# Kernel tuning notes

Measured on AMD Instinct MI355X. Metric: run time of the kernel, lower is better.

## Reference

```python
import jax, jax.numpy as jnp
import numpy as np

N, E, IN, HID, ADIM, EDIM, H = 20000, 320000, 128, 128, 16, 16, 2


def _lin(key, out_d, in_d, scale=0.05):
    kw, kb = jax.random.split(key)
    W = jax.random.normal(kw, (out_d, in_d), jnp.float32) * scale
    b = jax.random.normal(kb, (out_d,), jnp.float32) * scale
    return W, b


def _gat_params(key):
    k = jax.random.split(key, 4)
    Wl, bl = _lin(k[0], H * HID, HID)
    Wr, br = _lin(k[1], H * HID, HID)
    We = jax.random.normal(k[2], (H * HID, EDIM), jnp.float32) * 0.05  # lin_edge, no bias
    att = jax.random.normal(k[3], (1, H, HID), jnp.float32) * 0.05
    bias = jnp.zeros((HID,), jnp.float32)  # concat=False -> out bias of size HID
    return Wl, bl, Wr, br, We, att, bias


def setup_inputs() -> dict:
    key = jax.random.key(0)
    ks = jax.random.split(key, 16)
    inp = {}
    inp['x'] = jax.random.normal(ks[0], (N, IN), jnp.float32)
    inp['edge_index'] = jax.random.randint(ks[1], (2, E), 0, N, jnp.int64 if jax.config.jax_enable_x64 else jnp.int32)
    inp['edge_attr'] = jax.random.normal(ks[2], (E, EDIM), jnp.float32)
    inp['action'] = jax.random.normal(ks[3], (N, ADIM), jnp.float32)
    inp['inp_W'], inp['inp_b'] = _lin(ks[4], HID, IN)
    for i, name in enumerate(['s1', 's2', 'sa']):
        Wl, bl, Wr, br, We, att, bias = _gat_params(ks[5 + i])
        inp[f'{name}_Wl'], inp[f'{name}_bl'] = Wl, bl
        inp[f'{name}_Wr'], inp[f'{name}_br'] = Wr, br
        inp[f'{name}_We'], inp[f'{name}_att'], inp[f'{name}_bias'] = We, att, bias
    inp['ap_W'], inp['ap_b'] = _lin(ks[8], HID, ADIM)
    inp['g_W'], inp['g_b'] = _lin(ks[9], HID, HID)
    inp['be_W'], inp['be_b'] = _lin(ks[10], HID, HID)
    inp['q1_W'], inp['q1_b'] = _lin(ks[11], HID, HID)
    inp['q2_W'], inp['q2_b'] = _lin(ks[12], 1, HID)
    return inp


def gatv2(h, src, dst, ea, Wl, bl, Wr, br, We, att, bias):
    """PyG GATv2Conv, heads=H, concat=False (mean over heads), with edge_attr."""
    n = h.shape[0]
    xl = (h @ Wl.T + bl).reshape(n, H, HID)   # source transform
    xr = (h @ Wr.T + br).reshape(n, H, HID)   # destination transform
    em = (ea @ We.T).reshape(-1, H, HID)      # [E,H,C]
    m = jax.nn.leaky_relu(xl[src] + xr[dst] + em, 0.2)   # [E,H,C]
    logit = (m * att).sum(-1)                 # [E,H]
    lmax = jax.ops.segment_max(logit, dst, num_segments=n)
    w = jnp.exp(logit - lmax[dst])
    den = jax.ops.segment_sum(w, dst, num_segments=n)
    alpha = w / den[dst]                      # segment softmax over incoming edges
    out = jax.ops.segment_sum(alpha[..., None] * xl[src], dst, num_segments=n)  # [n,H,C]
    return out.mean(axis=1) + bias


def reference(x, edge_index, edge_attr, action, inp_W, inp_b,
              s1_Wl, s1_bl, s1_Wr, s1_br, s1_We, s1_att, s1_bias,
              s2_Wl, s2_bl, s2_Wr, s2_br, s2_We, s2_att, s2_bias,
              sa_Wl, sa_bl, sa_Wr, sa_br, sa_We, sa_att, sa_bias,
              ap_W, ap_b, g_W, g_b, be_W, be_b, q1_W, q1_b, q2_W, q2_b):
    src, dst = edge_index[0], edge_index[1]
    h = jax.nn.relu(x @ inp_W.T + inp_b)
    h = jax.nn.relu(gatv2(h, src, dst, edge_attr, s1_Wl, s1_bl, s1_Wr, s1_br, s1_We, s1_att, s1_bias))
    h = jax.nn.relu(gatv2(h, src, dst, edge_attr, s2_Wl, s2_bl, s2_Wr, s2_br, s2_We, s2_att, s2_bias))
    a = jax.nn.relu(action @ ap_W.T + ap_b)
    h = (a @ g_W.T + g_b) * h + (a @ be_W.T + be_b)   # FiLM modulation
    h = jax.nn.relu(gatv2(h, src, dst, edge_attr, sa_Wl, sa_bl, sa_Wr, sa_br, sa_We, sa_att, sa_bias))
    h = jax.nn.relu(h @ q1_W.T + q1_b)
    q_node = h @ q2_W.T + q2_b                         # [N,1]
    return q_node.mean(axis=0, keepdims=True)          # [1,1]
```

## Files before the change

### kernel.cpp

```cpp
#include <hip/hip_runtime.h>
#include <hip/hip_bf16.h>


typedef __attribute__((ext_vector_type(8))) short bf16x8;
typedef __attribute__((ext_vector_type(4))) float f32x4;
typedef __attribute__((ext_vector_type(2))) float f32x2;

#define ZERO8 ((bf16x8){0, 0, 0, 0, 0, 0, 0, 0})

__device__ __forceinline__ unsigned short f2bf(float f) {
    union { float f; unsigned int i; } v; v.f = f;
    unsigned int x = v.i;
    x += 0x7fffu + ((x >> 16) & 1u);
    return (unsigned short)(x >> 16);
}
__device__ __forceinline__ unsigned char f2fp8(float f) {
    return (unsigned char)(__builtin_amdgcn_cvt_pk_fp8_f32(f, f, 0, false) & 0xFF);
}
__device__ __forceinline__ void wave_lds_fence() {
    __builtin_amdgcn_wave_barrier();
    asm volatile("s_waitcnt lgkmcnt(0)" ::: "memory");
    __builtin_amdgcn_wave_barrier();
}

#define MAXCVT 16
struct CvtDescs {
    const float* src[MAXCVT];
    unsigned short* dst[MAXCVT];
    int off4[MAXCVT + 1];
    int cnt;
    int* deg; int ndeg4;
    int* ctr; float* col;
};
__global__ __launch_bounds__(256) void cvt_many_kernel(CvtDescs d) {
    const int tid = blockIdx.x * blockDim.x + threadIdx.x;
    const int stride = gridDim.x * blockDim.x;
    const int total = d.off4[d.cnt];
    for (int i = tid; i < total; i += stride) {
        int e = 0;
        while (d.off4[e + 1] <= i) ++e;
        const int j = i - d.off4[e];
        float4 v = ((const float4*)d.src[e])[j];
        ((ushort4*)d.dst[e])[j] = make_ushort4(f2bf(v.x), f2bf(v.y), f2bf(v.z), f2bf(v.w));
    }
    for (int i = tid; i < d.ndeg4; i += stride)
        ((int4*)d.deg)[i] = make_int4(0, 0, 0, 0);
    if (tid == 0) { *d.ctr = 0; *d.col = 0.f; }
}

__global__ void hist_kernel(const int* __restrict__ dst, int* __restrict__ deg, int n) {
    int i = blockIdx.x * blockDim.x + threadIdx.x;
    if (i < n) atomicAdd(&deg[dst[i]], 1);
}

__global__ __launch_bounds__(1024) void scan_kernel(const int* __restrict__ deg,
                                                    int* __restrict__ rowp,
                                                    int* __restrict__ cur, int n) {
    __shared__ int sums[1024];
    const int t = threadIdx.x;
    const int PER = 20;
    int base = t * PER;
    int local[PER];
    int run = 0;
#pragma unroll
    for (int i = 0; i < PER; ++i) {
        int v = (base + i < n) ? deg[base + i] : 0;
        local[i] = run; run += v;
    }
    sums[t] = run; __syncthreads();
    for (int off = 1; off < 1024; off <<= 1) {
        int v = (t >= off) ? sums[t - off] : 0;
        __syncthreads();
        sums[t] += v;
        __syncthreads();
    }
    int offs = (t > 0) ? sums[t - 1] : 0;
#pragma unroll
    for (int i = 0; i < PER; ++i) {
        int idx = base + i;
        if (idx < n) { int v = offs + local[i]; rowp[idx] = v; cur[idx] = v; }
    }
    if (t == 0) rowp[n] = sums[1023];
}

__global__ void scatter_kernel(const int* __restrict__ src, const int* __restrict__ dst,
                               int* __restrict__ cur, const float4* __restrict__ ea,
                               int* __restrict__ csrs, int* __restrict__ csrd,
                               ushort4* __restrict__ eacsr, int n) {
    int i = blockIdx.x * blockDim.x + threadIdx.x;
    if (i < n) {
        int d = dst[i];
        int p = atomicAdd(&cur[d], 1);
        csrs[p] = src[i];
        csrd[p] = d;
        const float4* er = ea + (size_t)i * 4;
        ushort4* eo = eacsr + (size_t)p * 4;
#pragma unroll
        for (int q = 0; q < 4; ++q) {
            float4 v = er[q];
            eo[q] = make_ushort4(f2bf(v.x), f2bf(v.y), f2bf(v.z), f2bf(v.w));
        }
    }
}

template <bool RELU, bool SPLIT, bool AF32>
__global__ __launch_bounds__(256) void gemm_mfma_kernel(
    const void* __restrict__ Ap, const unsigned short* __restrict__ W,
    const float* __restrict__ bias0, const float* __restrict__ bias1, int bsplit,
    unsigned short* __restrict__ Cbf, unsigned char* __restrict__ Cf8,
    int M, int N, int K) {
    __shared__ unsigned char ctile[SPLIT ? 128 * 64 : 64];
    const int t = threadIdx.x;
    const int wave = t >> 6, lane = t & 63;
    const int lo = lane & 15, quad = lane >> 4;
    const int m0 = blockIdx.y * 128 + wave * 32;
    const int n0 = blockIdx.x * 64;

    f32x4 acc[2][4];
#pragma unroll
    for (int i = 0; i < 2; ++i)
#pragma unroll
        for (int j = 0; j < 4; ++j) acc[i][j] = (f32x4){0.f, 0.f, 0.f, 0.f};

    for (int k0 = 0; k0 < K; k0 += 32) {
        bf16x8 af[2], bfr[4];
#pragma unroll
        for (int mi = 0; mi < 2; ++mi) {
            const int mb = m0 + mi * 16;
            if (mb >= M) { af[mi] = ZERO8; continue; }
            if (AF32) {
                const float* A = (const float*)Ap;
                float4 a0 = *(const float4*)(A + (size_t)(mb + lo) * K + k0 + quad * 8);
                float4 a1 = *(const float4*)(A + (size_t)(mb + lo) * K + k0 + quad * 8 + 4);
                bf16x8 f;
                f[0] = (short)f2bf(a0.x); f[1] = (short)f2bf(a0.y);
                f[2] = (short)f2bf(a0.z); f[3] = (short)f2bf(a0.w);
                f[4] = (short)f2bf(a1.x); f[5] = (short)f2bf(a1.y);
                f[6] = (short)f2bf(a1.z); f[7] = (short)f2bf(a1.w);
                af[mi] = f;
            } else {
                const unsigned short* A = (const unsigned short*)Ap;
                af[mi] = *(const bf16x8*)(A + (size_t)(mb + lo) * K + k0 + quad * 8);
            }
        }
#pragma unroll
        for (int ni = 0; ni < 4; ++ni)
            bfr[ni] = *(const bf16x8*)(W + (size_t)(n0 + ni * 16 + lo) * K + k0 + quad * 8);
#pragma unroll
        for (int mi = 0; mi < 2; ++mi)
#pragma unroll
            for (int ni = 0; ni < 4; ++ni)
                acc[mi][ni] = __builtin_amdgcn_mfma_f32_16x16x32_bf16(af[mi], bfr[ni], acc[mi][ni], 0, 0, 0);
    }

    float bn[4];
#pragma unroll
    for (int ni = 0; ni < 4; ++ni) {
        const int n = n0 + ni * 16 + lo;
        const float* bp = (n < bsplit) ? bias0 : bias1;
        const int bi = (n < bsplit) ? n : n - bsplit;
        bn[ni] = bp[bi];
    }
    if (SPLIT) {
#pragma unroll
        for (int mi = 0; mi < 2; ++mi) {
#pragma unroll
            for (int ni = 0; ni < 4; ++ni) {
                const int n = ni * 16 + lo;
#pragma unroll
                for (int r = 0; r < 4; ++r) {
                    float o = acc[mi][ni][r] + bn[ni];
                    if (RELU) o = fmaxf(o, 0.f);
                    ctile[(wave * 32 + mi * 16 + quad * 4 + r) * 64 + n] = f2fp8(o);
                }
            }
        }
        __syncthreads();
        const int row = t >> 1, half = t & 1;
        const int grow = blockIdx.y * 128 + row;
        if (grow < M) {
            const unsigned char* srcp = &ctile[row * 64 + half * 32];
            unsigned char* dstp = Cf8 + (size_t)grow * 512 + n0 + half * 32;
            *(int4*)(dstp) = *(const int4*)(srcp);
            *(int4*)(dstp + 16) = *(const int4*)(srcp + 16);
        }
    } else {
#pragma unroll
        for (int mi = 0; mi < 2; ++mi) {
            const int mb = m0 + mi * 16;
            if (mb >= M) continue;
#pragma unroll
            for (int ni = 0; ni < 4; ++ni) {
                const int n = n0 + ni * 16 + lo;
#pragma unroll
                for (int r = 0; r < 4; ++r) {
                    float o = acc[mi][ni][r] + bn[ni];
                    if (RELU) o = fmaxf(o, 0.f);
                    Cbf[(size_t)(mb + quad * 4 + r) * N + n] = f2bf(o);
                }
            }
        }
    }
}

__global__ __launch_bounds__(256) void gemm_film_kernel(
    const unsigned short* __restrict__ A, const unsigned short* __restrict__ Wg,
    const unsigned short* __restrict__ Wb, const float* __restrict__ gb,
    const float* __restrict__ bb, unsigned short* __restrict__ hbf, int M) {
    const int K = 128, N = 128;
    const int t = threadIdx.x;
    const int wave = t >> 6, lane = t & 63;
    const int lo = lane & 15, quad = lane >> 4;
    const int m0 = blockIdx.y * 128 + wave * 32;
    const int n0 = blockIdx.x * 64;

    f32x4 accg[2][4], accb[2][4];
#pragma unroll
    for (int i = 0; i < 2; ++i)
#pragma unroll
        for (int j = 0; j < 4; ++j) { accg[i][j] = (f32x4){0.f,0.f,0.f,0.f}; accb[i][j] = accg[i][j]; }

    for (int k0 = 0; k0 < 128; k0 += 32) {
        bf16x8 af[2], bg4[4];
#pragma unroll
        for (int mi = 0; mi < 2; ++mi) {
            const int mb = m0 + mi * 16;
            af[mi] = (mb < M) ? *(const bf16x8*)(A + (size_t)(mb + lo) * K + k0 + quad * 8)
                              : ZERO8;
        }
#pragma unroll
        for (int ni = 0; ni < 4; ++ni)
            bg4[ni] = *(const bf16x8*)(Wg + (size_t)(n0 + ni * 16 + lo) * K + k0 + quad * 8);
#pragma unroll
        for (int mi = 0; mi < 2; ++mi)
#pragma unroll
            for (int ni = 0; ni < 4; ++ni)
                accg[mi][ni] = __builtin_amdgcn_mfma_f32_16x16x32_bf16(af[mi], bg4[ni], accg[mi][ni], 0, 0, 0);
#pragma unroll
        for (int ni = 0; ni < 4; ++ni)
            bg4[ni] = *(const bf16x8*)(Wb + (size_t)(n0 + ni * 16 + lo) * K + k0 + quad * 8);
#pragma unroll
        for (int mi = 0; mi < 2; ++mi)
#pragma unroll
            for (int ni = 0; ni < 4; ++ni)
                accb[mi][ni] = __builtin_amdgcn_mfma_f32_16x16x32_bf16(af[mi], bg4[ni], accb[mi][ni], 0, 0, 0);
    }

#pragma unroll
    for (int mi = 0; mi < 2; ++mi) {
        const int mb = m0 + mi * 16;
        if (mb >= M) continue;
#pragma unroll
        for (int ni = 0; ni < 4; ++ni) {
            const int n = n0 + ni * 16 + lo;
            const float g = gb[n], b = bb[n];
#pragma unroll
            for (int r = 0; r < 4; ++r) {
                const size_t idx = (size_t)(mb + quad * 4 + r) * N + n;
                union { unsigned int i; float f; } hv; hv.i = (unsigned int)hbf[idx] << 16;
                hbf[idx] = f2bf((accg[mi][ni][r] + g) * hv.f + (accb[mi][ni][r] + b));
            }
        }
    }
}

__global__ __launch_bounds__(256) void gemm_q1_kernel(
    const unsigned short* __restrict__ A, const unsigned short* __restrict__ W,
    const float* __restrict__ q1b, const float* __restrict__ q2w,
    const float* __restrict__ q2b, float* __restrict__ outsum,
    float* __restrict__ outv, int* __restrict__ ctr,
    int M, int nblk, float invn) {
    const int K = 128;
    const int t = threadIdx.x;
    const int wave = t >> 6, lane = t & 63;
    const int lo = lane & 15, quad = lane >> 4;
    const int m0 = blockIdx.y * 128 + wave * 32;
    const int n0 = blockIdx.x * 64;
    __shared__ float red[4];

    f32x4 acc[2][4];
#pragma unroll
    for (int i = 0; i < 2; ++i)
#pragma unroll
        for (int j = 0; j < 4; ++j) acc[i][j] = (f32x4){0.f, 0.f, 0.f, 0.f};

    for (int k0 = 0; k0 < K; k0 += 32) {
        bf16x8 af[2], bfr[4];
#pragma unroll
        for (int mi = 0; mi < 2; ++mi) {
            const int mb = m0 + mi * 16;
            af[mi] = (mb < M) ? *(const bf16x8*)(A + (size_t)(mb + lo) * K + k0 + quad * 8)
                              : ZERO8;
        }
#pragma unroll
        for (int ni = 0; ni < 4; ++ni)
            bfr[ni] = *(const bf16x8*)(W + (size_t)(n0 + ni * 16 + lo) * K + k0 + quad * 8);
#pragma unroll
        for (int mi = 0; mi < 2; ++mi)
#pragma unroll
            for (int ni = 0; ni < 4; ++ni)
                acc[mi][ni] = __builtin_amdgcn_mfma_f32_16x16x32_bf16(af[mi], bfr[ni], acc[mi][ni], 0, 0, 0);
    }

    float partial = 0.f;
#pragma unroll
    for (int mi = 0; mi < 2; ++mi) {
        const int mb = m0 + mi * 16;
        if (mb >= M) continue;
#pragma unroll
        for (int ni = 0; ni < 4; ++ni) {
            const int n = n0 + ni * 16 + lo;
            const float b = q1b[n], w = q2w[n];
#pragma unroll
            for (int r = 0; r < 4; ++r)
                partial += fmaxf(acc[mi][ni][r] + b, 0.f) * w;
        }
    }
    partial += __shfl_xor(partial, 1);  partial += __shfl_xor(partial, 2);
    partial += __shfl_xor(partial, 4);  partial += __shfl_xor(partial, 8);
    partial += __shfl_xor(partial, 16); partial += __shfl_xor(partial, 32);
    if (lane == 0) red[wave] = partial;
    __syncthreads();
    if (t == 0) {
        atomicAdd(outsum, red[0] + red[1] + red[2] + red[3]);
        __threadfence();
        unsigned int d = atomicAdd((unsigned int*)ctr, 1u);
        if (d == (unsigned int)(nblk - 1)) {
            float s = atomicAdd(outsum, 0.f);
            outv[0] = s * invn + q2b[0];
        }
    }
}

template <int BK, bool RELU>
__global__ __launch_bounds__(256) void gemm_kernel(const float* __restrict__ A,
                                                   const float* __restrict__ W,
                                                   const float* __restrict__ bp,
                                                   unsigned short* __restrict__ Cbf,
                                                   int M, int N, int K) {
    __shared__ float As[BK][68];
    __shared__ float Ws[BK][68];
    const int t = threadIdx.x;
    const int m0 = blockIdx.y * 64;
    const int n0 = blockIdx.x * 64;
    const int tx = t & 15, ty = t >> 4;
    float acc[4][4];
#pragma unroll
    for (int i = 0; i < 4; ++i)
#pragma unroll
        for (int j = 0; j < 4; ++j) acc[i][j] = 0.f;

    for (int k0 = 0; k0 < K; k0 += BK) {
        const int r = t >> 2, cc = (t & 3) * 4;
        const int arow = m0 + r;
        float4 av = (arow < M) ? *(const float4*)(A + (size_t)arow * K + k0 + cc)
                               : make_float4(0.f, 0.f, 0.f, 0.f);
        As[cc + 0][r] = av.x; As[cc + 1][r] = av.y;
        As[cc + 2][r] = av.z; As[cc + 3][r] = av.w;
        float4 wv = *(const float4*)(W + (size_t)(n0 + r) * K + k0 + cc);
        Ws[cc + 0][r] = wv.x; Ws[cc + 1][r] = wv.y;
        Ws[cc + 2][r] = wv.z; Ws[cc + 3][r] = wv.w;
        __syncthreads();
#pragma unroll
        for (int k = 0; k < BK; ++k) {
            float4 a4 = *(const float4*)&As[k][ty * 4];
            float4 b4 = *(const float4*)&Ws[k][tx * 4];
            float a_[4] = {a4.x, a4.y, a4.z, a4.w};
            float b_[4] = {b4.x, b4.y, b4.z, b4.w};
#pragma unroll
            for (int i = 0; i < 4; ++i)
#pragma unroll
                for (int j = 0; j < 4; ++j) acc[i][j] += a_[i] * b_[j];
        }
        __syncthreads();
    }
    float4 bj = *(const float4*)(bp + n0 + tx * 4);
    float bb[4] = {bj.x, bj.y, bj.z, bj.w};
#pragma unroll
    for (int i = 0; i < 4; ++i) {
        int row = m0 + ty * 4 + i;
        if (row < M) {
            float o[4];
#pragma unroll
            for (int j = 0; j < 4; ++j) {
                o[j] = acc[i][j] + bb[j];
                if (RELU) o[j] = fmaxf(o[j], 0.f);
            }
            *(ushort4*)(Cbf + (size_t)row * N + n0 + tx * 4) =
                make_ushort4(f2bf(o[0]), f2bf(o[1]), f2bf(o[2]), f2bf(o[3]));
        }
    }
}

#define LSTR 272
__global__ __launch_bounds__(256, 4) void gat_logit_kernel(
    const unsigned char* __restrict__ xf8,
    const int* __restrict__ csrs, const int* __restrict__ csrd,
    const unsigned short* __restrict__ eacsr, const unsigned short* __restrict__ we16,
    const float* __restrict__ att, float* __restrict__ logit, int E) {
    __shared__ float attl[256];
    __shared__ __align__(16) unsigned char xls[4][16 * LSTR];
    __shared__ __align__(16) unsigned char xrs[4][16 * LSTR];
    const int tid = threadIdx.x;
    attl[tid] = att[tid];
    const int wave = tid >> 6, lane = tid & 63;
    const int lo = lane & 15, quad = lane >> 4;
    const int sr_row = lane >> 2, c16 = (lane & 3) * 16;

    bf16x8 wef[16];
#pragma unroll
    for (int t = 0; t < 16; ++t)
        wef[t] = (quad < 2) ? *(const bf16x8*)(we16 + (size_t)(t * 16 + lo) * 16 + quad * 8)
                            : ZERO8;
    __syncthreads();

    const int nb = (E + 15) / 16;
    const int wstride = gridDim.x * 4;
    const int trips = (nb + wstride - 1) / wstride;
    for (int it = 0; it < trips; ++it) {
        const int b = blockIdx.x * 4 + wave + it * wstride;
        if (b >= nb) break;
        const int p0 = b * 16;
        {
            const int pr = min(p0 + sr_row, E - 1);
            const int sr = csrs[pr], dr = csrd[pr];
            const unsigned char* xs = xf8 + (size_t)sr * 512 + c16;
            const unsigned char* xrp = xf8 + (size_t)dr * 512 + 256 + c16;
            unsigned char* ld = &xls[wave][sr_row * LSTR + c16];
            unsigned char* rd = &xrs[wave][sr_row * LSTR + c16];
#pragma unroll
            for (int j = 0; j < 4; ++j) {
                *(int4*)(ld + j * 64) = *(const int4*)(xs + j * 64);
                *(int4*)(rd + j * 64) = *(const int4*)(xrp + j * 64);
            }
        }
        wave_lds_fence();
        {
            const bool valid = (p0 + lo) < E;
            const int p = valid ? (p0 + lo) : (E - 1);
            const bf16x8 eaf = (quad < 2)
                ? *(const bf16x8*)(eacsr + (size_t)p * 16 + quad * 8) : ZERO8;
            float ph0 = 0.f, ph1 = 0.f;
#pragma unroll
            for (int t = 0; t < 16; ++t) {
                f32x4 D = __builtin_amdgcn_mfma_f32_16x16x32_bf16(
                    wef[t], eaf, (f32x4){0.f, 0.f, 0.f, 0.f}, 0, 0, 0);
                const int c0 = t * 16 + quad * 4;
                const unsigned int xlu = *(const unsigned int*)&xls[wave][lo * LSTR + c0];
                const unsigned int xru = *(const unsigned int*)&xrs[wave][lo * LSTR + c0];
                const f32x2 l01 = __builtin_amdgcn_cvt_pk_f32_fp8(xlu, false);
                const f32x2 l23 = __builtin_amdgcn_cvt_pk_f32_fp8(xlu, true);
                const f32x2 r01 = __builtin_amdgcn_cvt_pk_f32_fp8(xru, false);
                const f32x2 r23 = __builtin_amdgcn_cvt_pk_f32_fp8(xru, true);
                const float4 at4 = *(const float4*)&attl[c0];
                float vx = l01.x + r01.x + D[0];
                float vy = l01.y + r01.y + D[1];
                float vz = l23.x + r23.x + D[2];
                float vw = l23.y + r23.y + D[3];
                vx = fmaxf(vx, 0.2f * vx); vy = fmaxf(vy, 0.2f * vy);
                vz = fmaxf(vz, 0.2f * vz); vw = fmaxf(vw, 0.2f * vw);
                const float pt = vx * at4.x + vy * at4.y + vz * at4.z + vw * at4.w;
                if (t < 8) ph0 += pt; else ph1 += pt;
            }
            ph0 += __shfl_xor(ph0, 16); ph0 += __shfl_xor(ph0, 32);
            ph1 += __shfl_xor(ph1, 16); ph1 += __shfl_xor(ph1, 32);
            if (valid) {
                if (quad == 0) logit[p0 + lo] = __expf(fminf(ph0, 60.f));
                else if (quad == 1) logit[(size_t)E + p0 + lo] = __expf(fminf(ph1, 60.f));
            }
        }
        wave_lds_fence();
    }
}

__global__ __launch_bounds__(256) void gat_na_kernel(
    const unsigned char* __restrict__ xf8,
    const int* __restrict__ rowp, const int* __restrict__ csrs,
    const float* __restrict__ wgt, const float* __restrict__ bias,
    unsigned short* __restrict__ houtb, int nnodes, int E) {
    const int lane = threadIdx.x & 63;
    const int node = blockIdx.x * 4 + (threadIdx.x >> 6);
    if (node >= nnodes) return;
    const int rs = rowp[node], re = rowp[node + 1];
    const int h = lane >> 5;
    const float* lg = wgt + (size_t)h * E;

    float den = 0.f;
    float4 acc = make_float4(0.f, 0.f, 0.f, 0.f);
    for (int i = rs; i < re; i += 8) {
        int s[8]; float w[8]; unsigned int u[8];
#pragma unroll
        for (int k = 0; k < 8; ++k) {
            const int p = min(i + k, re - 1);
            s[k] = csrs[p];
            w[k] = (i + k < re) ? lg[p] : 0.f;
        }
#pragma unroll
        for (int k = 0; k < 8; ++k)
            u[k] = *(const unsigned int*)(xf8 + (size_t)s[k] * 512 + 4 * lane);
#pragma unroll
        for (int k = 0; k < 8; ++k) {
            const f32x2 p01 = __builtin_amdgcn_cvt_pk_f32_fp8(u[k], false);
            const f32x2 p23 = __builtin_amdgcn_cvt_pk_f32_fp8(u[k], true);
            den += w[k];
            acc.x += w[k] * p01.x; acc.y += w[k] * p01.y;
            acc.z += w[k] * p23.x; acc.w += w[k] * p23.y;
        }
    }
    const float inv = (re > rs) ? 1.f / den : 0.f;
    float ox = acc.x * inv, oy = acc.y * inv, oz = acc.z * inv, ow = acc.w * inv;
    ox += __shfl_xor(ox, 32); oy += __shfl_xor(oy, 32);
    oz += __shfl_xor(oz, 32); ow += __shfl_xor(ow, 32);
    if (lane < 32) {
        float4 bu = *(const float4*)(bias + 4 * lane);
        *(ushort4*)(houtb + (size_t)node * 128 + 4 * lane) = make_ushort4(
            f2bf(fmaxf(0.5f * ox + bu.x, 0.f)), f2bf(fmaxf(0.5f * oy + bu.y, 0.f)),
            f2bf(fmaxf(0.5f * oz + bu.z, 0.f)), f2bf(fmaxf(0.5f * ow + bu.w, 0.f)));
    }
}

extern "C" void kernel_launch(void* const* d_in, const int* in_sizes, int n_in,
                              void* d_out, int out_size, void* d_ws, size_t ws_size,
                              hipStream_t stream) {
    const int N = in_sizes[0] / 128;
    const int E = in_sizes[1] / 2;

    typedef const float* fp;
    fp x      = (fp)d_in[0];
    const int* ei = (const int*)d_in[1];
    fp ea     = (fp)d_in[2];
    fp action = (fp)d_in[3];
    fp inp_W  = (fp)d_in[4];
    fp inp_b  = (fp)d_in[5];
    fp ap_W = (fp)d_in[27], ap_b = (fp)d_in[28];
    fp g_W  = (fp)d_in[29], g_b  = (fp)d_in[30];
    fp be_W = (fp)d_in[31], be_b = (fp)d_in[32];
    fp q1_W = (fp)d_in[33], q1_b = (fp)d_in[34];
    fp q2_W = (fp)d_in[35], q2_b = (fp)d_in[36];

    char* base = (char*)d_ws;
    size_t off = 0;
    auto alloc = [&](size_t bytes) { char* p = base + off; off = (off + bytes + 255) & ~(size_t)255; return p; };
    unsigned char*  xf8 = (unsigned char*)alloc((size_t)N * 512);
    float* col  = (float*)alloc(128 * 4);
    int* ctr    = (int*)alloc(256);
    int* deg    = (int*)alloc((size_t)N * 4);
    int* rowp   = (int*)alloc((size_t)(N + 1) * 4);
    int* cur    = (int*)alloc((size_t)N * 4);
    int* csrs   = (int*)alloc((size_t)E * 4);
    int* csrd   = (int*)alloc((size_t)E * 4);
    unsigned short* eacsr = (unsigned short*)alloc((size_t)E * 16 * 2);
    float* wgt  = (float*)alloc((size_t)2 * E * 4);
    unsigned short* hbf = (unsigned short*)alloc((size_t)N * 128 * 2);
    unsigned short* abf = (unsigned short*)alloc((size_t)N * 128 * 2);
    unsigned short* wbf = (unsigned short*)alloc((262144 + 3 * 4096) * 2);
    (void)ws_size; (void)n_in; (void)out_size;

    unsigned short* winp = wbf;
    unsigned short* w1l  = wbf + 16384;
    unsigned short* w1r  = w1l + 32768;
    unsigned short* w2l  = w1r + 32768;
    unsigned short* w2r  = w2l + 32768;
    unsigned short* wal  = w2r + 32768;
    unsigned short* war  = wal + 32768;
    unsigned short* wg   = war + 32768;
    unsigned short* wbe  = wg + 16384;
    unsigned short* wq1  = wbe + 16384;
    unsigned short* wep1 = wq1 + 16384;
    unsigned short* wep2 = wep1 + 4096;
    unsigned short* wep3 = wep2 + 4096;

    const int* src = ei;
    const int* dst = ei + E;

    CvtDescs cd;
    int ce = 0, acc4 = 0;
    auto addc = [&](const float* s, unsigned short* d, int n) {
        cd.src[ce] = s; cd.dst[ce] = d; cd.off4[ce] = acc4; acc4 += n / 4; ++ce; };
    addc(inp_W, winp, 16384);
    addc((fp)d_in[6],  w1l, 32768); addc((fp)d_in[8],  w1r, 32768);
    addc((fp)d_in[13], w2l, 32768); addc((fp)d_in[15], w2r, 32768);
    addc((fp)d_in[20], wal, 32768); addc((fp)d_in[22], war, 32768);
    addc(g_W, wg, 16384); addc(be_W, wbe, 16384); addc(q1_W, wq1, 16384);
    addc((fp)d_in[10], wep1, 4096); addc((fp)d_in[17], wep2, 4096); addc((fp)d_in[24], wep3, 4096);
    cd.off4[ce] = acc4; cd.cnt = ce;
    cd.deg = deg; cd.ndeg4 = (N + 3) / 4;
    cd.ctr = ctr; cd.col = col;
    cvt_many_kernel<<<(acc4 + 255) / 256, 256, 0, stream>>>(cd);

    hist_kernel<<<(E + 255) / 256, 256, 0, stream>>>(dst, deg, E);
    scan_kernel<<<1, 1024, 0, stream>>>(deg, rowp, cur, N);
    scatter_kernel<<<(E + 255) / 256, 256, 0, stream>>>(src, dst, cur, (const float4*)ea,
                                                        csrs, csrd, (ushort4*)eacsr, E);

    const int my = (N + 127) / 128;
    const int nodeg = (N + 3) / 4;

    auto run_gat = [&](const unsigned short* wep, const float* at, const float* bi,
                       unsigned short* hb) {
        gat_logit_kernel<<<2500, 256, 0, stream>>>(xf8, csrs, csrd, eacsr, wep, at, wgt, E);
        gat_na_kernel<<<nodeg, 256, 0, stream>>>(xf8, rowp, csrs, wgt, bi, hb, N, E);
    };

    gemm_mfma_kernel<true, false, true><<<dim3(2, my), 256, 0, stream>>>(
        x, winp, inp_b, inp_b, 128, hbf, nullptr, N, 128, 128);

    gemm_mfma_kernel<false, true, false><<<dim3(8, my), 256, 0, stream>>>(
        hbf, w1l, (fp)d_in[7], (fp)d_in[9], 256, nullptr, xf8, N, 512, 128);
    run_gat(wep1, (fp)d_in[11], (fp)d_in[12], hbf);
    gemm_mfma_kernel<false, true, false><<<dim3(8, my), 256, 0, stream>>>(
        hbf, w2l, (fp)d_in[14], (fp)d_in[16], 256, nullptr, xf8, N, 512, 128);
    run_gat(wep2, (fp)d_in[18], (fp)d_in[19], hbf);

    gemm_kernel<16, true><<<dim3(2, (N + 63) / 64), 256, 0, stream>>>(
        action, ap_W, ap_b, abf, N, 128, 16);
    gemm_film_kernel<<<dim3(2, my), 256, 0, stream>>>(abf, wg, wbe, g_b, be_b, hbf, N);

    gemm_mfma_kernel<false, true, false><<<dim3(8, my), 256, 0, stream>>>(
        hbf, wal, (fp)d_in[21], (fp)d_in[23], 256, nullptr, xf8, N, 512, 128);
    run_gat(wep3, (fp)d_in[25], (fp)d_in[26], hbf);

    gemm_q1_kernel<<<dim3(2, my), 256, 0, stream>>>(
        hbf, wq1, q1_b, q2_W, q2_b, col, (float*)d_out, ctr, N, 2 * my, 1.0f / (float)N);
}
```

Measured before the change: 424.0 us.

## Fuse action projection into FiLM GEMM and trim gat_logit LDS and register use

```diff
diff --git a/kernel.cpp b/kernel.cpp
--- a/kernel.cpp
+++ b/kernel.cpp
@@ -204,15 +204,56 @@
 }
 
 __global__ __launch_bounds__(256) void gemm_film_kernel(
-    const unsigned short* __restrict__ A, const unsigned short* __restrict__ Wg,
-    const unsigned short* __restrict__ Wb, const float* __restrict__ gb,
-    const float* __restrict__ bb, unsigned short* __restrict__ hbf, int M) {
+    const float* __restrict__ action, const unsigned short* __restrict__ wap,
+    const float* __restrict__ apb,
+    const unsigned short* __restrict__ Wg, const unsigned short* __restrict__ Wb,
+    const float* __restrict__ gb, const float* __restrict__ bb,
+    unsigned short* __restrict__ hbf, int M) {
     const int K = 128, N = 128;
+    __shared__ __align__(16) unsigned short atile[128][136];
     const int t = threadIdx.x;
     const int wave = t >> 6, lane = t & 63;
     const int lo = lane & 15, quad = lane >> 4;
     const int m0 = blockIdx.y * 128 + wave * 32;
     const int n0 = blockIdx.x * 64;
+    const int r0 = wave * 32;
+
+    {
+        bf16x8 afa[2];
+#pragma unroll
+        for (int mi = 0; mi < 2; ++mi) {
+            const int row = m0 + mi * 16 + lo;
+            if (row < M && quad < 2) {
+                float4 a0 = *(const float4*)(action + (size_t)row * 16 + quad * 8);
+                float4 a1 = *(const float4*)(action + (size_t)row * 16 + quad * 8 + 4);
+                bf16x8 f;
+                f[0] = (short)f2bf(a0.x); f[1] = (short)f2bf(a0.y);
+                f[2] = (short)f2bf(a0.z); f[3] = (short)f2bf(a0.w);
+                f[4] = (short)f2bf(a1.x); f[5] = (short)f2bf(a1.y);
+                f[6] = (short)f2bf(a1.z); f[7] = (short)f2bf(a1.w);
+                afa[mi] = f;
+            } else afa[mi] = ZERO8;
+        }
+#pragma unroll
+        for (int nj = 0; nj < 8; ++nj) {
+            const bf16x8 bga = (quad < 2)
+                ? *(const bf16x8*)(wap + (size_t)(nj * 16 + lo) * 16 + quad * 8) : ZERO8;
+            f32x4 aa[2];
+#pragma unroll
+            for (int mi = 0; mi < 2; ++mi)
+                aa[mi] = __builtin_amdgcn_mfma_f32_16x16x32_bf16(
+                    afa[mi], bga, (f32x4){0.f, 0.f, 0.f, 0.f}, 0, 0, 0);
+            const int ch = nj * 16 + lo;
+            const float b = apb[ch];
+#pragma unroll
+            for (int mi = 0; mi < 2; ++mi)
+#pragma unroll
+                for (int r = 0; r < 4; ++r)
+                    atile[r0 + mi * 16 + quad * 4 + r][ch] =
+                        f2bf(fmaxf(aa[mi][r] + b, 0.f));
+        }
+    }
+    wave_lds_fence();
 
     f32x4 accg[2][4], accb[2][4];
 #pragma unroll
@@ -225,7 +266,7 @@
 #pragma unroll
         for (int mi = 0; mi < 2; ++mi) {
             const int mb = m0 + mi * 16;
-            af[mi] = (mb < M) ? *(const bf16x8*)(A + (size_t)(mb + lo) * K + k0 + quad * 8)
+            af[mi] = (mb < M) ? *(const bf16x8*)&atile[r0 + mi * 16 + lo][k0 + quad * 8]
                               : ZERO8;
         }
 #pragma unroll
@@ -332,86 +373,26 @@
     }
 }
 
-template <int BK, bool RELU>
-__global__ __launch_bounds__(256) void gemm_kernel(const float* __restrict__ A,
-                                                   const float* __restrict__ W,
-                                                   const float* __restrict__ bp,
-                                                   unsigned short* __restrict__ Cbf,
-                                                   int M, int N, int K) {
-    __shared__ float As[BK][68];
-    __shared__ float Ws[BK][68];
-    const int t = threadIdx.x;
-    const int m0 = blockIdx.y * 64;
-    const int n0 = blockIdx.x * 64;
-    const int tx = t & 15, ty = t >> 4;
-    float acc[4][4];
-#pragma unroll
-    for (int i = 0; i < 4; ++i)
-#pragma unroll
-        for (int j = 0; j < 4; ++j) acc[i][j] = 0.f;
-
-    for (int k0 = 0; k0 < K; k0 += BK) {
-        const int r = t >> 2, cc = (t & 3) * 4;
-        const int arow = m0 + r;
-        float4 av = (arow < M) ? *(const float4*)(A + (size_t)arow * K + k0 + cc)
-                               : make_float4(0.f, 0.f, 0.f, 0.f);
-        As[cc + 0][r] = av.x; As[cc + 1][r] = av.y;
-        As[cc + 2][r] = av.z; As[cc + 3][r] = av.w;
-        float4 wv = *(const float4*)(W + (size_t)(n0 + r) * K + k0 + cc);
-        Ws[cc + 0][r] = wv.x; Ws[cc + 1][r] = wv.y;
-        Ws[cc + 2][r] = wv.z; Ws[cc + 3][r] = wv.w;
-        __syncthreads();
-#pragma unroll
-        for (int k = 0; k < BK; ++k) {
-            float4 a4 = *(const float4*)&As[k][ty * 4];
-            float4 b4 = *(const float4*)&Ws[k][tx * 4];
-            float a_[4] = {a4.x, a4.y, a4.z, a4.w};
-            float b_[4] = {b4.x, b4.y, b4.z, b4.w};
-#pragma unroll
-            for (int i = 0; i < 4; ++i)
-#pragma unroll
-                for (int j = 0; j < 4; ++j) acc[i][j] += a_[i] * b_[j];
-        }
-        __syncthreads();
-    }
-    float4 bj = *(const float4*)(bp + n0 + tx * 4);
-    float bb[4] = {bj.x, bj.y, bj.z, bj.w};
-#pragma unroll
-    for (int i = 0; i < 4; ++i) {
-        int row = m0 + ty * 4 + i;
-        if (row < M) {
-            float o[4];
-#pragma unroll
-            for (int j = 0; j < 4; ++j) {
-                o[j] = acc[i][j] + bb[j];
-                if (RELU) o[j] = fmaxf(o[j], 0.f);
-            }
-            *(ushort4*)(Cbf + (size_t)row * N + n0 + tx * 4) =
-                make_ushort4(f2bf(o[0]), f2bf(o[1]), f2bf(o[2]), f2bf(o[3]));
-        }
-    }
-}
-
 #define LSTR 272
-__global__ __launch_bounds__(256, 4) void gat_logit_kernel(
+__global__ __launch_bounds__(256, 5) void gat_logit_kernel(
     const unsigned char* __restrict__ xf8,
     const int* __restrict__ csrs, const int* __restrict__ csrd,
     const unsigned short* __restrict__ eacsr, const unsigned short* __restrict__ we16,
     const float* __restrict__ att, float* __restrict__ logit, int E) {
     __shared__ float attl[256];
+    __shared__ __align__(16) unsigned short wefl[4096];
     __shared__ __align__(16) unsigned char xls[4][16 * LSTR];
-    __shared__ __align__(16) unsigned char xrs[4][16 * LSTR];
     const int tid = threadIdx.x;
     attl[tid] = att[tid];
+    {
+        const int4* ws = (const int4*)we16;
+        int4* wd = (int4*)wefl;
+        wd[tid] = ws[tid];
+        wd[tid + 256] = ws[tid + 256];
+    }
     const int wave = tid >> 6, lane = tid & 63;
     const int lo = lane & 15, quad = lane >> 4;
     const int sr_row = lane >> 2, c16 = (lane & 3) * 16;
-
-    bf16x8 wef[16];
-#pragma unroll
-    for (int t = 0; t < 16; ++t)
-        wef[t] = (quad < 2) ? *(const bf16x8*)(we16 + (size_t)(t * 16 + lo) * 16 + quad * 8)
-                            : ZERO8;
     __syncthreads();
 
     const int nb = (E + 15) / 16;
@@ -423,31 +404,31 @@
         const int p0 = b * 16;
         {
             const int pr = min(p0 + sr_row, E - 1);
-            const int sr = csrs[pr], dr = csrd[pr];
+            const int sr = csrs[pr];
             const unsigned char* xs = xf8 + (size_t)sr * 512 + c16;
-            const unsigned char* xrp = xf8 + (size_t)dr * 512 + 256 + c16;
             unsigned char* ld = &xls[wave][sr_row * LSTR + c16];
-            unsigned char* rd = &xrs[wave][sr_row * LSTR + c16];
-#pragma unroll
-            for (int j = 0; j < 4; ++j) {
+#pragma unroll
+            for (int j = 0; j < 4; ++j)
                 *(int4*)(ld + j * 64) = *(const int4*)(xs + j * 64);
-                *(int4*)(rd + j * 64) = *(const int4*)(xrp + j * 64);
-            }
         }
         wave_lds_fence();
         {
             const bool valid = (p0 + lo) < E;
             const int p = valid ? (p0 + lo) : (E - 1);
+            const int dr = csrd[p];
+            const unsigned char* xrbase = xf8 + (size_t)dr * 512 + 256;
             const bf16x8 eaf = (quad < 2)
                 ? *(const bf16x8*)(eacsr + (size_t)p * 16 + quad * 8) : ZERO8;
             float ph0 = 0.f, ph1 = 0.f;
 #pragma unroll
             for (int t = 0; t < 16; ++t) {
+                const bf16x8 wf = (quad < 2)
+                    ? *(const bf16x8*)&wefl[(t * 16 + lo) * 16 + quad * 8] : ZERO8;
                 f32x4 D = __builtin_amdgcn_mfma_f32_16x16x32_bf16(
-                    wef[t], eaf, (f32x4){0.f, 0.f, 0.f, 0.f}, 0, 0, 0);
+                    wf, eaf, (f32x4){0.f, 0.f, 0.f, 0.f}, 0, 0, 0);
                 const int c0 = t * 16 + quad * 4;
                 const unsigned int xlu = *(const unsigned int*)&xls[wave][lo * LSTR + c0];
-                const unsigned int xru = *(const unsigned int*)&xrs[wave][lo * LSTR + c0];
+                const unsigned int xru = *(const unsigned int*)(xrbase + c0);
                 const f32x2 l01 = __builtin_amdgcn_cvt_pk_f32_fp8(xlu, false);
                 const f32x2 l23 = __builtin_amdgcn_cvt_pk_f32_fp8(xlu, true);
                 const f32x2 r01 = __builtin_amdgcn_cvt_pk_f32_fp8(xru, false);
@@ -552,8 +533,7 @@
     unsigned short* eacsr = (unsigned short*)alloc((size_t)E * 16 * 2);
     float* wgt  = (float*)alloc((size_t)2 * E * 4);
     unsigned short* hbf = (unsigned short*)alloc((size_t)N * 128 * 2);
-    unsigned short* abf = (unsigned short*)alloc((size_t)N * 128 * 2);
-    unsigned short* wbf = (unsigned short*)alloc((262144 + 3 * 4096) * 2);
+    unsigned short* wbf = (unsigned short*)alloc((262144 + 3 * 4096 + 2048) * 2);
     (void)ws_size; (void)n_in; (void)out_size;
 
     unsigned short* winp = wbf;
@@ -569,6 +549,7 @@
     unsigned short* wep1 = wq1 + 16384;
     unsigned short* wep2 = wep1 + 4096;
     unsigned short* wep3 = wep2 + 4096;
+    unsigned short* wap  = wep3 + 4096;
 
     const int* src = ei;
     const int* dst = ei + E;
@@ -583,6 +564,7 @@
     addc((fp)d_in[20], wal, 32768); addc((fp)d_in[22], war, 32768);
     addc(g_W, wg, 16384); addc(be_W, wbe, 16384); addc(q1_W, wq1, 16384);
     addc((fp)d_in[10], wep1, 4096); addc((fp)d_in[17], wep2, 4096); addc((fp)d_in[24], wep3, 4096);
+    addc(ap_W, wap, 2048);
     cd.off4[ce] = acc4; cd.cnt = ce;
     cd.deg = deg; cd.ndeg4 = (N + 3) / 4;
     cd.ctr = ctr; cd.col = col;
@@ -612,9 +594,8 @@
         hbf, w2l, (fp)d_in[14], (fp)d_in[16], 256, nullptr, xf8, N, 512, 128);
     run_gat(wep2, (fp)d_in[18], (fp)d_in[19], hbf);
 
-    gemm_kernel<16, true><<<dim3(2, (N + 63) / 64), 256, 0, stream>>>(
-        action, ap_W, ap_b, abf, N, 128, 16);
-    gemm_film_kernel<<<dim3(2, my), 256, 0, stream>>>(abf, wg, wbe, g_b, be_b, hbf, N);
+    gemm_film_kernel<<<dim3(2, my), 256, 0, stream>>>(
+        action, wap, ap_b, wg, wbe, g_b, be_b, hbf, N);
 
     gemm_mfma_kernel<false, true, false><<<dim3(8, my), 256, 0, stream>>>(
         hbf, wal, (fp)d_in[21], (fp)d_in[23], 256, nullptr, xf8, N, 512, 128);
```

Result: slower. 764.8 us (+80.4%).
